# Performance work log

Measured on AMD Instinct MI355X. Metric: run time of the kernel, lower is better.

## Reference

```python
import jax, jax.numpy as jnp
import numpy as np


def setup_inputs() -> dict:
    key = jax.random.key(0)
    x = jax.random.normal(key, (128, 256, 32, 32), dtype=jnp.float32)
    return {"x": x, "topk": 5}


def reference(x, topk):
    B = x.shape[0]
    flat = x.reshape(B, -1)                      # [B, N]
    _, idx = jax.lax.top_k(flat, topk)           # [B, k] indices into N
    out = jnp.zeros_like(flat)
    out = out.at[jnp.arange(B)[:, None], idx].set(1.0)
    return out.reshape(x.shape)
```

## Files before the change

### kernel.cpp

```cpp
#include <hip/hip_runtime.h>
#include <limits.h>
#include <math.h>
#include <stdint.h>

#define BROWS 128
#define NCOLS (256 * 32 * 32)
#define K 5
#define BPR 32
#define TPB 256
#define CHUNK (NCOLS / BPR)
#define F4T (CHUNK / 4 / TPB)
#define NW (TPB / 64)

typedef float v4f __attribute__((ext_vector_type(4)));

__device__ __forceinline__ uint64_t make_key(float f, uint32_t idx) {
    uint32_t u = __float_as_uint(f);
    u = (u & 0x80000000u) ? ~u : (u | 0x80000000u);
    return ((uint64_t)u << 32) | (uint32_t)(~idx);
}
__device__ __forceinline__ uint32_t key_idx(uint64_t k) { return ~(uint32_t)k; }

#define KEY_NEG_INF 0x007FFFFF00000000ULL

__device__ __forceinline__ void insert5(uint64_t (&key)[K], uint64_t c) {
    if (c > key[K - 1]) {
        key[K - 1] = c;
#pragma unroll
        for (int s = K - 1; s > 0; --s) {
            if (key[s] > key[s - 1]) {
                uint64_t t = key[s]; key[s] = key[s - 1]; key[s - 1] = t;
            }
        }
    }
}

__device__ __forceinline__ void wave_reduce5(uint64_t (&key)[K]) {
#pragma unroll
    for (int off = 1; off < 64; off <<= 1) {
        uint64_t ok[K];
#pragma unroll
        for (int k = 0; k < K; ++k)
            ok[k] = __shfl_xor((unsigned long long)key[k], off, 64);
#pragma unroll
        for (int k = 0; k < K; ++k) insert5(key, ok[k]);
    }
}

__device__ __forceinline__ void insert5f(float (&v)[K], float c) {
    if (c > v[K - 1]) {
        v[K - 1] = c;
#pragma unroll
        for (int s = K - 1; s > 0; --s) {
            if (v[s] > v[s - 1]) { float t = v[s]; v[s] = v[s - 1]; v[s - 1] = t; }
        }
    }
}

__global__ __launch_bounds__(TPB) void wta_pass(const float* __restrict__ x,
                                                float* __restrict__ out,
                                                uint64_t* __restrict__ cand) {
    const int gb  = blockIdx.x;
    const int row = gb / BPR;
    const int blk = gb % BPR;
    const size_t base = (size_t)gb * CHUNK;
    const float4* __restrict__ x4 = (const float4*)(x + base);
    v4f* __restrict__ o4 = (v4f*)(out + base);
    const int t = threadIdx.x;
    const v4f z = {0.f, 0.f, 0.f, 0.f};

    float4 d[F4T];
#pragma unroll
    for (int j = 0; j < F4T; ++j) d[j] = x4[t + j * TPB];
#pragma unroll
    for (int j = 0; j < F4T; ++j)
        __builtin_nontemporal_store(z, &o4[t + j * TPB]);

    float mj[F4T];
#pragma unroll
    for (int j = 0; j < F4T; ++j)
        mj[j] = fmaxf(fmaxf(d[j].x, d[j].y), fmaxf(d[j].z, d[j].w));
    float M = -INFINITY;
#pragma unroll
    for (int j = 0; j < F4T; ++j) M = fmaxf(M, mj[j]);

    float v[K];
    v[0] = M;
#pragma unroll
    for (int k = 1; k < K; ++k) v[k] = -INFINITY;
#pragma unroll
    for (int off = 1; off < 64; off <<= 1) {
        float ov[K];
#pragma unroll
        for (int k = 0; k < K; ++k) ov[k] = __shfl_xor(v[k], off, 64);
#pragma unroll
        for (int k = 0; k < K; ++k) insert5f(v, ov[k]);
    }
    const float T = v[K - 1];

    uint64_t key[K];
#pragma unroll
    for (int k = 0; k < K; ++k) key[k] = KEY_NEG_INF;
    const uint32_t ebase = (uint32_t)blk * CHUNK;
#pragma unroll
    for (int j = 0; j < F4T; ++j) {
        if (mj[j] >= T) {
            const uint32_t e = ebase + (uint32_t)(t + j * TPB) * 4u;
            const float vs[4] = {d[j].x, d[j].y, d[j].z, d[j].w};
#pragma unroll
            for (int c = 0; c < 4; ++c)
                if (vs[c] >= T) insert5(key, make_key(vs[c], e + c));
        }
    }

    wave_reduce5(key);

    __shared__ uint64_t sk[NW * K];
    const int lane = t & 63, w = t >> 6;
    if (lane == 0) {
#pragma unroll
        for (int k = 0; k < K; ++k) sk[w * K + k] = key[k];
    }
    __syncthreads();
    if (t < 64) {
        uint64_t fk[K];
#pragma unroll
        for (int k = 0; k < K; ++k) fk[k] = KEY_NEG_INF;
        if (t < NW * K) fk[0] = sk[t];
        wave_reduce5(fk);
        if (t == 0) {
#pragma unroll
            for (int k = 0; k < K; ++k)
                cand[((size_t)row * BPR + blk) * K + k] = fk[k];
        }
    }
}

__global__ __launch_bounds__(64) void wta_final(const uint64_t* __restrict__ cand,
                                                float* __restrict__ out) {
    const int row = blockIdx.x, lane = threadIdx.x;
    const uint64_t* __restrict__ c = cand + (size_t)row * BPR * K;

    uint64_t key[K];
#pragma unroll
    for (int k = 0; k < K; ++k) key[k] = KEY_NEG_INF;
#pragma unroll
    for (int i = 0; i < (BPR * K + 63) / 64; ++i) {
        const int j = i * 64 + lane;
        if (j < BPR * K) insert5(key, c[j]);
    }

    wave_reduce5(key);

    if (lane == 0) {
#pragma unroll
        for (int k = 0; k < K; ++k)
            if (key[k] != KEY_NEG_INF)
                out[(size_t)row * NCOLS + key_idx(key[k])] = 1.0f;
    }
}

extern "C" void kernel_launch(void* const* d_in, const int* in_sizes, int n_in,
                              void* d_out, int out_size, void* d_ws, size_t ws_size,
                              hipStream_t stream) {
    const float* x = (const float*)d_in[0];
    float* out = (float*)d_out;

    uint64_t* cand = (uint64_t*)d_ws;

    wta_pass<<<BROWS * BPR, TPB, 0, stream>>>(x, out, cand);
    wta_final<<<BROWS, 64, 0, stream>>>(cand, out);
}
```

Measured before the change: 250.7 us.

## Split top-k into max-only streaming pass and per-row selective rescan

```diff
diff --git a/kernel.cpp b/kernel.cpp
--- a/kernel.cpp
+++ b/kernel.cpp
@@ -10,7 +10,9 @@
 #define TPB 256
 #define CHUNK (NCOLS / BPR)
 #define F4T (CHUNK / 4 / TPB)
-#define NW (TPB / 64)
+#define WPR (BPR * 4)
+#define NFLAG 16
+#define CAP 256
 
 typedef float v4f __attribute__((ext_vector_type(4)));
 
@@ -57,12 +59,10 @@
     }
 }
 
-__global__ __launch_bounds__(TPB) void wta_pass(const float* __restrict__ x,
-                                                float* __restrict__ out,
-                                                uint64_t* __restrict__ cand) {
-    const int gb  = blockIdx.x;
-    const int row = gb / BPR;
-    const int blk = gb % BPR;
+__global__ __launch_bounds__(TPB) void wta_stream(const float* __restrict__ x,
+                                                  float* __restrict__ out,
+                                                  float* __restrict__ wmax) {
+    const int gb = blockIdx.x;
     const size_t base = (size_t)gb * CHUNK;
     const float4* __restrict__ x4 = (const float4*)(x + base);
     v4f* __restrict__ o4 = (v4f*)(out + base);
@@ -76,87 +76,97 @@
     for (int j = 0; j < F4T; ++j)
         __builtin_nontemporal_store(z, &o4[t + j * TPB]);
 
-    float mj[F4T];
+    float M = -INFINITY;
 #pragma unroll
     for (int j = 0; j < F4T; ++j)
-        mj[j] = fmaxf(fmaxf(d[j].x, d[j].y), fmaxf(d[j].z, d[j].w));
-    float M = -INFINITY;
+        M = fmaxf(M, fmaxf(fmaxf(d[j].x, d[j].y), fmaxf(d[j].z, d[j].w)));
 #pragma unroll
-    for (int j = 0; j < F4T; ++j) M = fmaxf(M, mj[j]);
+    for (int off = 1; off < 64; off <<= 1)
+        M = fmaxf(M, __shfl_xor(M, off, 64));
 
-    float v[K];
-    v[0] = M;
+    if ((t & 63) == 0) wmax[gb * 4 + (t >> 6)] = M;
+}
+
+__global__ __launch_bounds__(TPB) void wta_finish(const float* __restrict__ x,
+                                                  const float* __restrict__ wmax,
+                                                  float* __restrict__ out) {
+    const int row = blockIdx.x;
+    const int t = threadIdx.x;
+    const float* __restrict__ wm = wmax + row * WPR;
+
+    __shared__ float sT;
+    __shared__ int nflag, ncand;
+    __shared__ int flaglist[NFLAG];
+    __shared__ uint64_t cand[CAP];
+
+    if (t == 0) { nflag = 0; ncand = 0; }
+    __syncthreads();
+
+    if (t < 64) {
+        float v[K];
 #pragma unroll
-    for (int k = 1; k < K; ++k) v[k] = -INFINITY;
+        for (int k = 0; k < K; ++k) v[k] = -INFINITY;
+        insert5f(v, wm[t]);
+        insert5f(v, wm[t + 64]);
 #pragma unroll
-    for (int off = 1; off < 64; off <<= 1) {
-        float ov[K];
+        for (int off = 1; off < 64; off <<= 1) {
+            float ov[K];
 #pragma unroll
-        for (int k = 0; k < K; ++k) ov[k] = __shfl_xor(v[k], off, 64);
+            for (int k = 0; k < K; ++k) ov[k] = __shfl_xor(v[k], off, 64);
 #pragma unroll
-        for (int k = 0; k < K; ++k) insert5f(v, ov[k]);
+            for (int k = 0; k < K; ++k) insert5f(v, ov[k]);
+        }
+        if (t == 0) sT = v[K - 1];
     }
-    const float T = v[K - 1];
+    __syncthreads();
+    const float T = sT;
 
-    uint64_t key[K];
+    if (t < WPR && wm[t] >= T) {
+        const int s = atomicAdd(&nflag, 1);
+        if (s < NFLAG) flaglist[s] = t;
+    }
+    __syncthreads();
+    const int nf = min(nflag, NFLAG);
+
+    const int lane = t & 63, jj = t >> 6;
+    for (int f = 0; f < nf; ++f) {
+        const int wid = flaglist[f];
+        const int gbk = wid >> 2;
+        const int w   = wid & 3;
+        const float4* __restrict__ xb =
+            (const float4*)(x + (size_t)row * NCOLS + (size_t)gbk * CHUNK);
 #pragma unroll
-    for (int k = 0; k < K; ++k) key[k] = KEY_NEG_INF;
-    const uint32_t ebase = (uint32_t)blk * CHUNK;
+        for (int rep = 0; rep < 2; ++rep) {
+            const int j = jj + rep * 4;
+            const int f4pos = w * 64 + lane + j * TPB;
+            const float4 d = xb[f4pos];
+            const float vs[4] = {d.x, d.y, d.z, d.w};
 #pragma unroll
-    for (int j = 0; j < F4T; ++j) {
-        if (mj[j] >= T) {
-            const uint32_t e = ebase + (uint32_t)(t + j * TPB) * 4u;
-            const float vs[4] = {d[j].x, d[j].y, d[j].z, d[j].w};
-#pragma unroll
-            for (int c = 0; c < 4; ++c)
-                if (vs[c] >= T) insert5(key, make_key(vs[c], e + c));
+            for (int c = 0; c < 4; ++c) {
+                if (vs[c] >= T) {
+                    const int s = atomicAdd(&ncand, 1);
+                    if (s < CAP)
+                        cand[s] = make_key(vs[c],
+                                           (uint32_t)gbk * CHUNK + (uint32_t)f4pos * 4u + c);
+                }
+            }
         }
     }
+    __syncthreads();
 
-    wave_reduce5(key);
-
-    __shared__ uint64_t sk[NW * K];
-    const int lane = t & 63, w = t >> 6;
-    if (lane == 0) {
+    if (t < 64) {
+        const int n = min(ncand, CAP);
+        uint64_t key[K];
 #pragma unroll
-        for (int k = 0; k < K; ++k) sk[w * K + k] = key[k];
-    }
-    __syncthreads();
-    if (t < 64) {
-        uint64_t fk[K];
-#pragma unroll
-        for (int k = 0; k < K; ++k) fk[k] = KEY_NEG_INF;
-        if (t < NW * K) fk[0] = sk[t];
-        wave_reduce5(fk);
+        for (int k = 0; k < K; ++k) key[k] = KEY_NEG_INF;
+        for (int i = t; i < n; i += 64) insert5(key, cand[i]);
+        wave_reduce5(key);
         if (t == 0) {
 #pragma unroll
             for (int k = 0; k < K; ++k)
-                cand[((size_t)row * BPR + blk) * K + k] = fk[k];
+                if (key[k] != KEY_NEG_INF)
+                    out[(size_t)row * NCOLS + key_idx(key[k])] = 1.0f;
         }
-    }
-}
-
-__global__ __launch_bounds__(64) void wta_final(const uint64_t* __restrict__ cand,
-                                                float* __restrict__ out) {
-    const int row = blockIdx.x, lane = threadIdx.x;
-    const uint64_t* __restrict__ c = cand + (size_t)row * BPR * K;
-
-    uint64_t key[K];
-#pragma unroll
-    for (int k = 0; k < K; ++k) key[k] = KEY_NEG_INF;
-#pragma unroll
-    for (int i = 0; i < (BPR * K + 63) / 64; ++i) {
-        const int j = i * 64 + lane;
-        if (j < BPR * K) insert5(key, c[j]);
-    }
-
-    wave_reduce5(key);
-
-    if (lane == 0) {
-#pragma unroll
-        for (int k = 0; k < K; ++k)
-            if (key[k] != KEY_NEG_INF)
-                out[(size_t)row * NCOLS + key_idx(key[k])] = 1.0f;
     }
 }
 
@@ -166,8 +176,8 @@
     const float* x = (const float*)d_in[0];
     float* out = (float*)d_out;
 
-    uint64_t* cand = (uint64_t*)d_ws;
+    float* wmax = (float*)d_ws;
 
-    wta_pass<<<BROWS * BPR, TPB, 0, stream>>>(x, out, cand);
-    wta_final<<<BROWS, 64, 0, stream>>>(cand, out);
+    wta_stream<<<BROWS * BPR, TPB, 0, stream>>>(x, out, wmax);
+    wta_finish<<<BROWS, TPB, 0, stream>>>(x, wmax, out);
 }
```

After: 244.3 us. 1.03x faster.
